# Kernel tuning notes

Measured on AMD Instinct MI355X. Metric: run time of the kernel, lower is better.

## Reference

```python
import jax, jax.numpy as jnp
import numpy as np

N = 10000
E = 320000
D_IN = 512
D_OUT = 256


def setup_inputs() -> dict:
    key = jax.random.key(0)
    ks = jax.random.split(key, 10)
    x = jax.random.normal(ks[0], (N, D_IN), dtype=jnp.float32)
    edge_index = jax.random.randint(ks[1], (2, E), 0, N, dtype=jnp.int64)
    s_in = 1.0 / np.sqrt(D_IN)
    s_out = 1.0 / np.sqrt(D_OUT)
    W0 = jax.random.uniform(ks[2], (D_IN, D_OUT), minval=-s_in, maxval=s_in, dtype=jnp.float32)
    b0 = jax.random.uniform(ks[3], (D_OUT,), minval=-s_in, maxval=s_in, dtype=jnp.float32)
    Wl1 = jax.random.uniform(ks[4], (D_OUT, D_OUT), minval=-s_out, maxval=s_out, dtype=jnp.float32)
    bl1 = jax.random.uniform(ks[5], (D_OUT,), minval=-s_out, maxval=s_out, dtype=jnp.float32)
    Wr1 = jax.random.uniform(ks[6], (D_OUT, D_OUT), minval=-s_out, maxval=s_out, dtype=jnp.float32)
    Wl2 = jax.random.uniform(ks[7], (D_OUT, D_OUT), minval=-s_out, maxval=s_out, dtype=jnp.float32)
    bl2 = jax.random.uniform(ks[8], (D_OUT,), minval=-s_out, maxval=s_out, dtype=jnp.float32)
    Wr2 = jax.random.uniform(ks[9], (D_OUT, D_OUT), minval=-s_out, maxval=s_out, dtype=jnp.float32)
    return {"x": x, "edge_index": edge_index, "W0": W0, "b0": b0,
            "Wl1": Wl1, "bl1": bl1, "Wr1": Wr1,
            "Wl2": Wl2, "bl2": bl2, "Wr2": Wr2}


def _sage_conv(h, src, dst, Wl, bl, Wr):
    # mean aggregation over incoming edges: msg j->i uses h[src], summed at dst
    msg = h[src]                                        # [E, D]
    agg = jax.ops.segment_sum(msg, dst, num_segments=N)  # [N, D]
    deg = jax.ops.segment_sum(jnp.ones((msg.shape[0],), h.dtype), dst, num_segments=N)
    mean = agg / jnp.maximum(deg, 1.0)[:, None]
    return mean @ Wl + bl + h @ Wr


def reference(x, edge_index, W0, b0, Wl1, bl1, Wr1, Wl2, bl2, Wr2):
    src, dst = edge_index[0], edge_index[1]
    h = x @ W0 + b0                 # lin; dropout = identity (eval mode)
    out1 = jax.nn.relu(_sage_conv(h, src, dst, Wl1, bl1, Wr1)) + h
    out2 = _sage_conv(out1, src, dst, Wl2, bl2, Wr2) + out1
    return (out1, out2)
```

## Files before the change

kernel.cpp:

```cpp
#include <hip/hip_runtime.h>
#include <cstdint>

#define N_NODES 10000
#define N_EDGES 320000
#define DIN 512
#define DOUT 256
#define KDIM 512

using short8 = __attribute__((ext_vector_type(8))) short;
using f32x4  = __attribute__((ext_vector_type(4))) float;
typedef unsigned short ushort_t;

static __device__ __forceinline__ unsigned short f2bf(float f) {
  unsigned u = __builtin_bit_cast(unsigned, f);
  u += 0x7fffu + ((u >> 16) & 1u);
  return (unsigned short)(u >> 16);
}
static __device__ __forceinline__ float bf2f(unsigned short s) {
  unsigned u = ((unsigned)s) << 16;
  return __builtin_bit_cast(float, u);
}

static __device__ __forceinline__ int detect64(const unsigned* ei) {
  unsigned z = 0;
  #pragma unroll
  for (int i = 1; i < 32; i += 2) z |= ei[i];
  return z == 0u;
}
static __device__ __forceinline__ int load_idx(const unsigned* ei, int i, int is64) {
  return is64 ? (int)ei[2 * i] : (int)ei[i];
}

#define B_EDGE 1250
#define B_W    1536
#define B_X    5000
__global__ __launch_bounds__(256) void prep_all(
    const unsigned* __restrict__ ei, int* __restrict__ deg,
    const float* __restrict__ x, ushort_t* __restrict__ xb,
    const float* __restrict__ W0,
    const float* __restrict__ Wl1, const float* __restrict__ Wr1,
    const float* __restrict__ Wl2, const float* __restrict__ Wr2,
    ushort_t* __restrict__ W0T, ushort_t* __restrict__ WT1,
    ushort_t* __restrict__ WT2) {
  int b = blockIdx.x;
  if (b < B_EDGE) {
    int is64 = detect64(ei);
    int e = b * 256 + threadIdx.x;
    int d = load_idx(ei, N_EDGES + e, is64);
    atomicAdd(&deg[d], 1);
  } else if (b < B_EDGE + B_W) {
    int g = (b - B_EDGE) * 256 + threadIdx.x;
    int mat = g >> 17;
    int r = g & 131071;
    int n = r >> 9, k = r & 511;
    float v;
    ushort_t* dst;
    if (mat == 0)      { v = W0[k * 256 + n]; dst = W0T; }
    else if (mat == 1) { v = (k < 256) ? Wl1[k * 256 + n] : Wr1[(k - 256) * 256 + n]; dst = WT1; }
    else               { v = (k < 256) ? Wl2[k * 256 + n] : Wr2[(k - 256) * 256 + n]; dst = WT2; }
    dst[r] = f2bf(v);
  } else {
    int g = (b - B_EDGE - B_W) * 256 + threadIdx.x;
    float4 f = *(const float4*)(x + (size_t)g * 4);
    uint2 o;
    o.x = (unsigned)f2bf(f.x) | ((unsigned)f2bf(f.y) << 16);
    o.y = (unsigned)f2bf(f.z) | ((unsigned)f2bf(f.w) << 16);
    *(uint2*)(xb + (size_t)g * 4) = o;
  }
}

__global__ __launch_bounds__(1024) void scan_k(const int* __restrict__ deg,
                                               int* __restrict__ rowp,
                                               int* __restrict__ cursor) {
  __shared__ int buf[1024];
  int tid = threadIdx.x;
  int loc[10];
  int s = 0;
  #pragma unroll
  for (int q = 0; q < 10; ++q) {
    int i = tid * 10 + q;
    int v = (i < N_NODES) ? deg[i] : 0;
    loc[q] = s;
    s += v;
  }
  buf[tid] = s;
  __syncthreads();
  #pragma unroll
  for (int off = 1; off < 1024; off <<= 1) {
    int t = (tid >= off) ? buf[tid - off] : 0;
    __syncthreads();
    buf[tid] += t;
    __syncthreads();
  }
  int excl = buf[tid] - s;
  #pragma unroll
  for (int q = 0; q < 10; ++q) {
    int i = tid * 10 + q;
    if (i < N_NODES) {
      int val = excl + loc[q];
      rowp[i] = val;
      cursor[i] = val;
    }
  }
  if (tid == 1023) rowp[N_NODES] = buf[1023];
}

__global__ __launch_bounds__(256) void scatter_k(const unsigned* __restrict__ ei,
                                                 int* __restrict__ cursor,
                                                 int* __restrict__ srcs) {
  int is64 = detect64(ei);
  int e = blockIdx.x * 256 + threadIdx.x;
  int d = load_idx(ei, N_EDGES + e, is64);
  int s = load_idx(ei, e, is64);
  int pos = atomicAdd(&cursor[d], 1);
  srcs[pos] = s;
}

__global__ __launch_bounds__(256) void agg_mean(const ushort_t* __restrict__ h,
                                                const int* __restrict__ rowp,
                                                const int* __restrict__ srcs,
                                                ushort_t* __restrict__ mean) {
  int node = blockIdx.x * 4 + (threadIdx.x >> 6);
  int lane = threadIdx.x & 63;
  if (node >= N_NODES) return;
  int beg = rowp[node], end = rowp[node + 1];
  float a0 = 0.f, a1 = 0.f, a2 = 0.f, a3 = 0.f;
  int j = beg;
  for (; j + 4 <= end; j += 4) {
    int s0 = srcs[j], s1 = srcs[j + 1], s2 = srcs[j + 2], s3 = srcs[j + 3];
    uint2 u0 = *(const uint2*)(h + (size_t)s0 * 512 + lane * 4);
    uint2 u1 = *(const uint2*)(h + (size_t)s1 * 512 + lane * 4);
    uint2 u2 = *(const uint2*)(h + (size_t)s2 * 512 + lane * 4);
    uint2 u3 = *(const uint2*)(h + (size_t)s3 * 512 + lane * 4);
    a0 += bf2f(u0.x & 0xffff) + bf2f(u1.x & 0xffff) + bf2f(u2.x & 0xffff) + bf2f(u3.x & 0xffff);
    a1 += bf2f(u0.x >> 16)    + bf2f(u1.x >> 16)    + bf2f(u2.x >> 16)    + bf2f(u3.x >> 16);
    a2 += bf2f(u0.y & 0xffff) + bf2f(u1.y & 0xffff) + bf2f(u2.y & 0xffff) + bf2f(u3.y & 0xffff);
    a3 += bf2f(u0.y >> 16)    + bf2f(u1.y >> 16)    + bf2f(u2.y >> 16)    + bf2f(u3.y >> 16);
  }
  for (; j < end; ++j) {
    int s0 = srcs[j];
    uint2 u0 = *(const uint2*)(h + (size_t)s0 * 512 + lane * 4);
    a0 += bf2f(u0.x & 0xffff);
    a1 += bf2f(u0.x >> 16);
    a2 += bf2f(u0.y & 0xffff);
    a3 += bf2f(u0.y >> 16);
  }
  int d = end - beg;
  float inv = 1.0f / (float)(d > 1 ? d : 1);
  a0 *= inv; a1 *= inv; a2 *= inv; a3 *= inv;
  uint2 o;
  o.x = (unsigned)f2bf(a0) | ((unsigned)f2bf(a1) << 16);
  o.y = (unsigned)f2bf(a2) | ((unsigned)f2bf(a3) << 16);
  *(uint2*)(mean + (size_t)node * 512 + lane * 4) = o;
}

template<int DO_RELU, int HAS_ADD, int HAS_OUTB>
__global__ __launch_bounds__(256) void gemm_k(
    const ushort_t* __restrict__ A, const ushort_t* __restrict__ BT,
    const float* __restrict__ bias, const float* __restrict__ addend,
    float* __restrict__ outF, ushort_t* __restrict__ outB, int outB_ld, int M) {
  __shared__ ushort_t As[64 * 72];
  __shared__ ushort_t Bs[64 * 72];

  const int tid  = threadIdx.x;
  const int lane = tid & 63;
  const int w    = tid >> 6;
  const int wm   = (w & 1) * 32;
  const int wn   = (w >> 1) * 32;
  const int bm   = blockIdx.x * 64;
  const int bn   = blockIdx.y * 64;

  f32x4 acc[2][2] = {};

  const int srow = tid >> 3;
  const int scol = (tid & 7) * 8;

  for (int kt = 0; kt < KDIM; kt += 64) {
    __syncthreads();
    #pragma unroll
    for (int p = 0; p < 2; ++p) {
      int r = p * 32 + srow;
      int gm = bm + r;
      uint4 av = make_uint4(0, 0, 0, 0);
      if (gm < M) av = *(const uint4*)(A + (size_t)gm * KDIM + kt + scol);
      *(uint4*)&As[r * 72 + scol] = av;
      uint4 bv = *(const uint4*)(BT + (size_t)(bn + r) * KDIM + kt + scol);
      *(uint4*)&Bs[r * 72 + scol] = bv;
    }
    __syncthreads();

    const int mrow = lane & 15;
    const int k8   = (lane >> 4) * 8;
    #pragma unroll
    for (int s = 0; s < 2; ++s) {
      const int kc = s * 32 + k8;
      short8 a[2], b[2];
      #pragma unroll
      for (int mi = 0; mi < 2; ++mi)
        a[mi] = *(const short8*)&As[(wm + mi * 16 + mrow) * 72 + kc];
      #pragma unroll
      for (int ni = 0; ni < 2; ++ni)
        b[ni] = *(const short8*)&Bs[(wn + ni * 16 + mrow) * 72 + kc];
      #pragma unroll
      for (int mi = 0; mi < 2; ++mi)
        #pragma unroll
        for (int ni = 0; ni < 2; ++ni)
          acc[mi][ni] = __builtin_amdgcn_mfma_f32_16x16x32_bf16(a[mi], b[ni], acc[mi][ni], 0, 0, 0);
    }
  }

  const int cq   = lane >> 4;
  const int ccol = lane & 15;
  #pragma unroll
  for (int ni = 0; ni < 2; ++ni) {
    int gcol = bn + wn + ni * 16 + ccol;
    float bv = bias[gcol];
    #pragma unroll
    for (int mi = 0; mi < 2; ++mi) {
      #pragma unroll
      for (int r = 0; r < 4; ++r) {
        int grow = bm + wm + mi * 16 + cq * 4 + r;
        if (grow < M) {
          float v = acc[mi][ni][r] + bv;
          if (DO_RELU) v = fmaxf(v, 0.f);
          if (HAS_ADD) v += addend[(size_t)grow * DOUT + gcol];
          outF[(size_t)grow * DOUT + gcol] = v;
          if (HAS_OUTB) outB[(size_t)grow * outB_ld + gcol] = f2bf(v);
        }
      }
    }
  }
}

extern "C" void kernel_launch(void* const* d_in, const int* in_sizes, int n_in,
                              void* d_out, int out_size, void* d_ws, size_t ws_size,
                              hipStream_t stream) {
  const float*    x   = (const float*)d_in[0];
  const unsigned* ei  = (const unsigned*)d_in[1];
  const float*    W0  = (const float*)d_in[2];
  const float*    b0  = (const float*)d_in[3];
  const float*    Wl1 = (const float*)d_in[4];
  const float*    bl1 = (const float*)d_in[5];
  const float*    Wr1 = (const float*)d_in[6];
  const float*    Wl2 = (const float*)d_in[7];
  const float*    bl2 = (const float*)d_in[8];
  const float*    Wr2 = (const float*)d_in[9];

  char* ws = (char*)d_ws;
  size_t off = 0;
  auto alloc = [&](size_t bytes) {
    char* p = ws + off;
    off += (bytes + 255) & ~(size_t)255;
    return p;
  };
  ushort_t* xb  = (ushort_t*)alloc((size_t)N_NODES * 512 * 2);
  ushort_t* c1  = (ushort_t*)alloc((size_t)N_NODES * 512 * 2);
  ushort_t* c2  = (ushort_t*)alloc((size_t)N_NODES * 512 * 2);
  float*    hf  = (float*)alloc((size_t)N_NODES * DOUT * 4);
  ushort_t* W0T = (ushort_t*)alloc(256 * 512 * 2);
  ushort_t* WT1 = (ushort_t*)alloc(256 * 512 * 2);
  ushort_t* WT2 = (ushort_t*)alloc(256 * 512 * 2);
  int* deg    = (int*)alloc(N_NODES * 4);
  int* rowp   = (int*)alloc((N_NODES + 1) * 4);
  int* cursor = (int*)alloc(N_NODES * 4);
  int* srcs   = (int*)alloc((size_t)N_EDGES * 4);

  float* out1 = (float*)d_out;
  float* out2 = out1 + (size_t)N_NODES * DOUT;

  hipMemsetAsync(deg, 0, N_NODES * 4, stream);
  prep_all<<<B_EDGE + B_W + B_X, 256, 0, stream>>>(ei, deg, x, xb,
                                                   W0, Wl1, Wr1, Wl2, Wr2,
                                                   W0T, WT1, WT2);
  scan_k<<<1, 1024, 0, stream>>>(deg, rowp, cursor);
  scatter_k<<<N_EDGES / 256, 256, 0, stream>>>(ei, cursor, srcs);

  dim3 ggrid((N_NODES + 63) / 64, 4);
  gemm_k<0, 0, 1><<<ggrid, 256, 0, stream>>>(xb, W0T, b0, nullptr,
                                             hf, c1 + 256, 512, N_NODES);
  agg_mean<<<(N_NODES + 3) / 4, 256, 0, stream>>>(c1 + 256, rowp, srcs, c1);
  gemm_k<1, 1, 1><<<ggrid, 256, 0, stream>>>(c1, WT1, bl1, hf,
                                             out1, c2 + 256, 512, N_NODES);
  agg_mean<<<(N_NODES + 3) / 4, 256, 0, stream>>>(c2 + 256, rowp, srcs, c2);
  gemm_k<0, 1, 0><<<ggrid, 256, 0, stream>>>(c2, WT2, bl2, out1,
                                             out2, nullptr, 0, N_NODES);
}
```

Measured before the change: 237.3 us.

## Rewrite GEMMs as B-panel-resident kernels with split-A inputs and bf16 residuals

Replaces the 64x64 LDS-tiled GEMM with a kernel that loads the full 64x512 weight panel into shared memory once. A is read straight from global into registers, and each block covers 128 rows. The concatenated [mean|h] buffers are split into separate 256-wide bf16 arrays read through a SPLIT_A path, and the fp32 h residual buffer is dropped in favour of bf16 addends. The intent is to cut syncs, LDS traffic and residual bandwidth, at the cost of about 66KB of LDS per block (lower occupancy), uncached direct global A loads, and extra rounding from the bf16 residual.

```diff
diff --git a/kernel.cpp b/kernel.cpp
--- a/kernel.cpp
+++ b/kernel.cpp
@@ -5,7 +5,6 @@
 #define N_EDGES 320000
 #define DIN 512
 #define DOUT 256
-#define KDIM 512
 
 using short8 = __attribute__((ext_vector_type(8))) short;
 using f32x4  = __attribute__((ext_vector_type(4))) float;
@@ -128,10 +127,10 @@
   int j = beg;
   for (; j + 4 <= end; j += 4) {
     int s0 = srcs[j], s1 = srcs[j + 1], s2 = srcs[j + 2], s3 = srcs[j + 3];
-    uint2 u0 = *(const uint2*)(h + (size_t)s0 * 512 + lane * 4);
-    uint2 u1 = *(const uint2*)(h + (size_t)s1 * 512 + lane * 4);
-    uint2 u2 = *(const uint2*)(h + (size_t)s2 * 512 + lane * 4);
-    uint2 u3 = *(const uint2*)(h + (size_t)s3 * 512 + lane * 4);
+    uint2 u0 = *(const uint2*)(h + (size_t)s0 * 256 + lane * 4);
+    uint2 u1 = *(const uint2*)(h + (size_t)s1 * 256 + lane * 4);
+    uint2 u2 = *(const uint2*)(h + (size_t)s2 * 256 + lane * 4);
+    uint2 u3 = *(const uint2*)(h + (size_t)s3 * 256 + lane * 4);
     a0 += bf2f(u0.x & 0xffff) + bf2f(u1.x & 0xffff) + bf2f(u2.x & 0xffff) + bf2f(u3.x & 0xffff);
     a1 += bf2f(u0.x >> 16)    + bf2f(u1.x >> 16)    + bf2f(u2.x >> 16)    + bf2f(u3.x >> 16);
     a2 += bf2f(u0.y & 0xffff) + bf2f(u1.y & 0xffff) + bf2f(u2.y & 0xffff) + bf2f(u3.y & 0xffff);
@@ -139,7 +138,7 @@
   }
   for (; j < end; ++j) {
     int s0 = srcs[j];
-    uint2 u0 = *(const uint2*)(h + (size_t)s0 * 512 + lane * 4);
+    uint2 u0 = *(const uint2*)(h + (size_t)s0 * 256 + lane * 4);
     a0 += bf2f(u0.x & 0xffff);
     a1 += bf2f(u0.x >> 16);
     a2 += bf2f(u0.y & 0xffff);
@@ -151,81 +150,82 @@
   uint2 o;
   o.x = (unsigned)f2bf(a0) | ((unsigned)f2bf(a1) << 16);
   o.y = (unsigned)f2bf(a2) | ((unsigned)f2bf(a3) << 16);
-  *(uint2*)(mean + (size_t)node * 512 + lane * 4) = o;
-}
-
-template<int DO_RELU, int HAS_ADD, int HAS_OUTB>
-__global__ __launch_bounds__(256) void gemm_k(
-    const ushort_t* __restrict__ A, const ushort_t* __restrict__ BT,
-    const float* __restrict__ bias, const float* __restrict__ addend,
-    float* __restrict__ outF, ushort_t* __restrict__ outB, int outB_ld, int M) {
-  __shared__ ushort_t As[64 * 72];
-  __shared__ ushort_t Bs[64 * 72];
+  *(uint2*)(mean + (size_t)node * 256 + lane * 4) = o;
+}
+
+template<int DO_RELU, int HAS_ADD, int HAS_OUTF, int HAS_OUTB, int SPLIT_A>
+__global__ __launch_bounds__(256) void gemm_pan(
+    const ushort_t* __restrict__ A0, const ushort_t* __restrict__ A1,
+    const ushort_t* __restrict__ BT, const float* __restrict__ bias,
+    const ushort_t* __restrict__ addB,
+    float* __restrict__ outF, ushort_t* __restrict__ outB, int M) {
+  __shared__ ushort_t Bs[64 * 520];
 
   const int tid  = threadIdx.x;
   const int lane = tid & 63;
   const int w    = tid >> 6;
-  const int wm   = (w & 1) * 32;
-  const int wn   = (w >> 1) * 32;
-  const int bm   = blockIdx.x * 64;
   const int bn   = blockIdx.y * 64;
-
-  f32x4 acc[2][2] = {};
-
-  const int srow = tid >> 3;
-  const int scol = (tid & 7) * 8;
-
-  for (int kt = 0; kt < KDIM; kt += 64) {
-    __syncthreads();
-    #pragma unroll
-    for (int p = 0; p < 2; ++p) {
-      int r = p * 32 + srow;
-      int gm = bm + r;
-      uint4 av = make_uint4(0, 0, 0, 0);
-      if (gm < M) av = *(const uint4*)(A + (size_t)gm * KDIM + kt + scol);
-      *(uint4*)&As[r * 72 + scol] = av;
-      uint4 bv = *(const uint4*)(BT + (size_t)(bn + r) * KDIM + kt + scol);
-      *(uint4*)&Bs[r * 72 + scol] = bv;
-    }
-    __syncthreads();
-
-    const int mrow = lane & 15;
-    const int k8   = (lane >> 4) * 8;
+  const int mbase = blockIdx.x * 128 + w * 32;
+
+  #pragma unroll
+  for (int i = 0; i < 16; ++i) {
+    int c = i * 256 + tid;
+    int row = c >> 6;
+    int c8  = (c & 63) * 8;
+    uint4 bv = *(const uint4*)(BT + (size_t)(bn + row) * 512 + c8);
+    *(uint4*)&Bs[row * 520 + c8] = bv;
+  }
+  __syncthreads();
+
+  f32x4 acc[2][4] = {};
+  const int mrow = lane & 15;
+  const int k8   = (lane >> 4) * 8;
+
+  #pragma unroll
+  for (int kt = 0; kt < 512; kt += 32) {
+    const ushort_t* Asrc;
+    int acol, ald;
+    if (SPLIT_A) {
+      if (kt < 256) { Asrc = A0; acol = kt; } else { Asrc = A1; acol = kt - 256; }
+      ald = 256;
+    } else {
+      Asrc = A0; acol = kt; ald = 512;
+    }
+    short8 a[2], b[4];
     #pragma unroll
     for (int s = 0; s < 2; ++s) {
-      const int kc = s * 32 + k8;
-      short8 a[2], b[2];
+      int row = mbase + s * 16 + mrow;
+      short8 av = {};
+      if (row < M) av = *(const short8*)(Asrc + (size_t)row * ald + acol + k8);
+      a[s] = av;
+    }
+    #pragma unroll
+    for (int ni = 0; ni < 4; ++ni)
+      b[ni] = *(const short8*)&Bs[(ni * 16 + mrow) * 520 + kt + k8];
+    #pragma unroll
+    for (int s = 0; s < 2; ++s)
       #pragma unroll
-      for (int mi = 0; mi < 2; ++mi)
-        a[mi] = *(const short8*)&As[(wm + mi * 16 + mrow) * 72 + kc];
-      #pragma unroll
-      for (int ni = 0; ni < 2; ++ni)
-        b[ni] = *(const short8*)&Bs[(wn + ni * 16 + mrow) * 72 + kc];
-      #pragma unroll
-      for (int mi = 0; mi < 2; ++mi)
-        #pragma unroll
-        for (int ni = 0; ni < 2; ++ni)
-          acc[mi][ni] = __builtin_amdgcn_mfma_f32_16x16x32_bf16(a[mi], b[ni], acc[mi][ni], 0, 0, 0);
-    }
+      for (int ni = 0; ni < 4; ++ni)
+        acc[s][ni] = __builtin_amdgcn_mfma_f32_16x16x32_bf16(a[s], b[ni], acc[s][ni], 0, 0, 0);
   }
 
   const int cq   = lane >> 4;
   const int ccol = lane & 15;
   #pragma unroll
-  for (int ni = 0; ni < 2; ++ni) {
-    int gcol = bn + wn + ni * 16 + ccol;
+  for (int ni = 0; ni < 4; ++ni) {
+    int gcol = bn + ni * 16 + ccol;
     float bv = bias[gcol];
     #pragma unroll
-    for (int mi = 0; mi < 2; ++mi) {
+    for (int s = 0; s < 2; ++s) {
       #pragma unroll
       for (int r = 0; r < 4; ++r) {
-        int grow = bm + wm + mi * 16 + cq * 4 + r;
+        int grow = mbase + s * 16 + cq * 4 + r;
         if (grow < M) {
-          float v = acc[mi][ni][r] + bv;
+          float v = acc[s][ni][r] + bv;
           if (DO_RELU) v = fmaxf(v, 0.f);
-          if (HAS_ADD) v += addend[(size_t)grow * DOUT + gcol];
-          outF[(size_t)grow * DOUT + gcol] = v;
-          if (HAS_OUTB) outB[(size_t)grow * outB_ld + gcol] = f2bf(v);
+          if (HAS_ADD) v += bf2f(addB[(size_t)grow * DOUT + gcol]);
+          if (HAS_OUTF) outF[(size_t)grow * DOUT + gcol] = v;
+          if (HAS_OUTB) outB[(size_t)grow * DOUT + gcol] = f2bf(v);
         }
       }
     }
@@ -254,9 +254,9 @@
     return p;
   };
   ushort_t* xb  = (ushort_t*)alloc((size_t)N_NODES * 512 * 2);
-  ushort_t* c1  = (ushort_t*)alloc((size_t)N_NODES * 512 * 2);
-  ushort_t* c2  = (ushort_t*)alloc((size_t)N_NODES * 512 * 2);
-  float*    hf  = (float*)alloc((size_t)N_NODES * DOUT * 4);
+  ushort_t* hb  = (ushort_t*)alloc((size_t)N_NODES * 256 * 2);
+  ushort_t* o1b = (ushort_t*)alloc((size_t)N_NODES * 256 * 2);
+  ushort_t* mb  = (ushort_t*)alloc((size_t)N_NODES * 256 * 2);
   ushort_t* W0T = (ushort_t*)alloc(256 * 512 * 2);
   ushort_t* WT1 = (ushort_t*)alloc(256 * 512 * 2);
   ushort_t* WT2 = (ushort_t*)alloc(256 * 512 * 2);
@@ -275,13 +275,13 @@
   scan_k<<<1, 1024, 0, stream>>>(deg, rowp, cursor);
   scatter_k<<<N_EDGES / 256, 256, 0, stream>>>(ei, cursor, srcs);
 
-  dim3 ggrid((N_NODES + 63) / 64, 4);
-  gemm_k<0, 0, 1><<<ggrid, 256, 0, stream>>>(xb, W0T, b0, nullptr,
-                                             hf, c1 + 256, 512, N_NODES);
-  agg_mean<<<(N_NODES + 3) / 4, 256, 0, stream>>>(c1 + 256, rowp, srcs, c1);
-  gemm_k<1, 1, 1><<<ggrid, 256, 0, stream>>>(c1, WT1, bl1, hf,
-                                             out1, c2 + 256, 512, N_NODES);
-  agg_mean<<<(N_NODES + 3) / 4, 256, 0, stream>>>(c2 + 256, rowp, srcs, c2);
-  gemm_k<0, 1, 0><<<ggrid, 256, 0, stream>>>(c2, WT2, bl2, out1,
-                                             out2, nullptr, 0, N_NODES);
-}
+  dim3 ggrid((N_NODES + 127) / 128, 4);
+  gemm_pan<0, 0, 0, 1, 0><<<ggrid, 256, 0, stream>>>(xb, nullptr, W0T, b0, nullptr,
+                                                     nullptr, hb, N_NODES);
+  agg_mean<<<(N_NODES + 3) / 4, 256, 0, stream>>>(hb, rowp, srcs, mb);
+  gemm_pan<1, 1, 1, 1, 1><<<ggrid, 256, 0, stream>>>(mb, hb, WT1, bl1, hb,
+                                                     out1, o1b, N_NODES);
+  agg_mean<<<(N_NODES + 3) / 4, 256, 0, stream>>>(o1b, rowp, srcs, mb);
+  gemm_pan<0, 1, 1, 0, 1><<<ggrid, 256, 0, stream>>>(mb, o1b, WT2, bl2, o1b,
+                                                     out2, nullptr, N_NODES);
+}
```

Measured after the change: 233.9 us. About the same (-1.5%).
